# Optimization experiments

Hardware: AMD Instinct MI355X
Metric: run time of the kernel (lower is better)

## Reference

```python
import jax, jax.numpy as jnp
import numpy as np

B, T, C, H = 2, 2048, 1024, 16  # batch, seq (== block_size), n_embd, n_head
HD = C // H  # head dim


def setup_inputs() -> dict:
    key = jax.random.key(0)
    k1, k2, k3 = jax.random.split(key, 3)
    x = jax.random.normal(k1, (B, T, C), dtype=jnp.float32)
    w_attn = jax.random.normal(k2, (C, 3 * C), dtype=jnp.float32) * (1.0 / np.sqrt(C))
    b_attn = jnp.zeros((3 * C,), dtype=jnp.float32)
    w_proj = jax.random.normal(k3, (C, C), dtype=jnp.float32) * (1.0 / np.sqrt(C))
    b_proj = jnp.zeros((C,), dtype=jnp.float32)
    return {"x": x, "w_attn": w_attn, "b_attn": b_attn, "w_proj": w_proj, "b_proj": b_proj}


def reference(x, w_attn, b_attn, w_proj, b_proj):
    # qkv projection: [B,T,3C]
    qkv = x @ w_attn + b_attn
    q, k, v = jnp.split(qkv, 3, axis=-1)
    # -> [B,H,T,HD]
    def to_heads(t):
        return t.reshape(B, T, H, HD).transpose(0, 2, 1, 3)
    q, k, v = to_heads(q), to_heads(k), to_heads(v)
    scale = 1.0 / np.sqrt(HD).astype(np.float32)
    # att: [B,H,T,T]
    att = jnp.einsum("bhqd,bhkd->bhqk", q, k) * scale
    causal = jnp.tril(jnp.ones((T, T), dtype=bool))
    att = jnp.where(causal[None, None], att, -jnp.inf)
    att = jax.nn.softmax(att, axis=-1)
    # y: [B,H,T,HD] -> [B,T,C]
    y = jnp.einsum("bhqk,bhkd->bhqd", att, v)
    y = y.transpose(0, 2, 1, 3).reshape(B, T, C)
    return y @ w_proj + b_proj
```

## Files before the change

kernel.cpp:

```cpp
#include <hip/hip_runtime.h>
#include <stdint.h>

#define Bb 2
#define Tt 2048
#define Cc 1024
#define Hh 16
#define HD 64
#define C3 3072

typedef __bf16 bf16x8 __attribute__((ext_vector_type(8)));
typedef float  f32x4  __attribute__((ext_vector_type(4)));
typedef unsigned short u16;
typedef u16 u16x8 __attribute__((ext_vector_type(8)));
typedef u16 u16x4 __attribute__((ext_vector_type(4)));

#define SCALE2 0.18033688f

__device__ __forceinline__ u16 f2bf(float f) {
  union { float f; unsigned u; } v; v.f = f;
  return (u16)((v.u + 0x7fffu + ((v.u >> 16) & 1u)) >> 16);
}
__device__ __forceinline__ float bf2f(u16 a) {
  union { unsigned u; float f; } v; v.u = ((unsigned)a) << 16; return v.f;
}

__device__ __forceinline__ void gl2lds16(const void* g, void* s) {
  __builtin_amdgcn_global_load_lds(
      (__attribute__((address_space(1))) void*)(g),
      (__attribute__((address_space(3))) void*)(s), 16, 0, 0);
}

__device__ __forceinline__ bf16x8 ldb8(const u16* p) {
  return __builtin_bit_cast(bf16x8, *(const u16x8*)p);
}

template <int N>
__device__ __forceinline__ void vmwait() {
  asm volatile("s_waitcnt vmcnt(%0)" :: "n"(N) : "memory");
}
__device__ __forceinline__ void barrier_nodrain() {
  __builtin_amdgcn_s_barrier();
  __builtin_amdgcn_sched_barrier(0);
}

__global__ __launch_bounds__(256)
void prep_kernel(const float* __restrict__ x, const float* __restrict__ w_attn,
                 const float* __restrict__ w_proj, u16* __restrict__ xb,
                 u16* __restrict__ wat, u16* __restrict__ wpt) {
  __shared__ u16 tile[64][65];
  const int blk = blockIdx.x;
  const int tid = threadIdx.x;
  if (blk < 4096) {
    int i = blk * 256 + tid;
    float4 v = ((const float4*)x)[i];
    u16x4 o = { f2bf(v.x), f2bf(v.y), f2bf(v.z), f2bf(v.w) };
    ((u16x4*)xb)[i] = o;
    return;
  }
  const float* in; u16* out; int R, C, c0, r0;
  if (blk < 4096 + 768) {
    int t = blk - 4096;
    in = w_attn; out = wat; R = 1024; C = 3072;
    c0 = (t % 48) * 64; r0 = (t / 48) * 64;
  } else {
    int t = blk - 4864;
    in = w_proj; out = wpt; R = 1024; C = 1024;
    c0 = (t & 15) * 64; r0 = (t >> 4) * 64;
  }
  int xx = tid & 63, yy = tid >> 6;
  #pragma unroll
  for (int rr = yy; rr < 64; rr += 4)
    tile[rr][xx] = f2bf(in[(size_t)(r0 + rr) * C + c0 + xx]);
  __syncthreads();
  #pragma unroll
  for (int rr = yy; rr < 64; rr += 4)
    out[(size_t)(c0 + rr) * R + r0 + xx] = tile[xx][rr];
}

template <int MODE, int BN, int MINW>
__global__ __launch_bounds__(256, MINW)
void gemm_bt(const u16* __restrict__ A, const u16* __restrict__ Bt,
             const float* __restrict__ bias, void* __restrict__ Cout,
             u16* __restrict__ Vt, int M, int N, int K) {
  __shared__ u16 As[3][128 * 32];
  __shared__ u16 Bs[3][BN * 32];
  constexpr int JT = BN / 32;
  constexpr int NB = BN / 128 + 1;
  constexpr int L  = 2 + NB;
  const int tid = threadIdx.x;
  const int ln  = tid & 63;
  const int w   = tid >> 6;
  const int wm  = w >> 1, wn = w & 1;
  const int l15 = ln & 15, lq = ln >> 4;
  const int swz2 = (l15 >> 1) & 3;
  const int m0 = blockIdx.y * 128, n0 = blockIdx.x * BN;

  int aoff[2], boff[NB];
  #pragma unroll
  for (int i = 0; i < 2; ++i) {
    int s = i * 256 + tid;
    int row = s >> 2, cg = (s & 3) ^ ((s >> 3) & 3);
    aoff[i] = (m0 + row) * K + cg * 8;
  }
  #pragma unroll
  for (int i = 0; i < NB; ++i) {
    int s = i * 256 + tid;
    int row = s >> 2, cg = (s & 3) ^ ((s >> 3) & 3);
    boff[i] = (n0 + row) * K + cg * 8;
  }

  f32x4 acc[4][JT];
  #pragma unroll
  for (int i = 0; i < 4; ++i)
    #pragma unroll
    for (int j = 0; j < JT; ++j)
      acc[i][j] = (f32x4){0.f, 0.f, 0.f, 0.f};

  const int NK = K >> 5;

  auto STAGE = [&](int buf, int t) {
    const int k0 = t * 32;
    #pragma unroll
    for (int i = 0; i < 2; ++i)
      gl2lds16(A + aoff[i] + k0, (char*)As[buf] + (size_t)(i * 256 + w * 64) * 16);
    #pragma unroll
    for (int i = 0; i < NB; ++i)
      gl2lds16(Bt + boff[i] + k0, (char*)Bs[buf] + (size_t)(i * 256 + w * 64) * 16);
  };

  STAGE(0, 0);
  if (NK > 1) STAGE(1, 1);

  int cur = 0;
  for (int it = 0; it < NK; ++it) {
    if (it + 1 < NK) vmwait<L>(); else vmwait<0>();
    barrier_nodrain();
    if (it + 2 < NK) STAGE(cur == 0 ? 2 : cur - 1, it + 2);
    const u16* AsB = As[cur];
    const u16* BsB = Bs[cur];
    bf16x8 af[4], bfr[JT];
    #pragma unroll
    for (int i = 0; i < 4; ++i)
      af[i] = ldb8(&AsB[(wm * 64 + i * 16 + l15) * 32 + ((lq ^ swz2) * 8)]);
    #pragma unroll
    for (int j = 0; j < JT; ++j)
      bfr[j] = ldb8(&BsB[(wn * (BN / 2) + j * 16 + l15) * 32 + ((lq ^ swz2) * 8)]);
    #pragma unroll
    for (int i = 0; i < 4; ++i)
      #pragma unroll
      for (int j = 0; j < JT; ++j)
        acc[i][j] = __builtin_amdgcn_mfma_f32_16x16x32_bf16(af[i], bfr[j], acc[i][j], 0, 0, 0);
    cur = (cur == 2) ? 0 : cur + 1;
  }

  if (MODE == 1 && n0 >= 2048) {
    #pragma unroll
    for (int i = 0; i < 4; ++i) {
      int rowb = m0 + wm * 64 + i * 16 + lq * 4;
      int b_ = rowb >> 11, t0 = rowb & 2047;
      int tl = t0 & 63;
      int c = tl >> 4, ll = (tl >> 2) & 3;
      int pos0 = (c >> 1) * 32 + ll * 8 + (c & 1) * 4;
      size_t tdst = (size_t)(t0 & ~63) + pos0;
      #pragma unroll
      for (int j = 0; j < JT; ++j) {
        int col = n0 + wn * (BN / 2) + j * 16 + l15;
        int hd = col - 2048;
        float bsv = bias[col];
        u16x4 pk;
        #pragma unroll
        for (int r = 0; r < 4; ++r) pk[r] = f2bf(acc[i][j][r] + bsv);
        *(u16x4*)&Vt[(size_t)(b_ * 1024 + hd) * Tt + tdst] = pk;
      }
    }
  } else {
    const int ldc = (MODE == 1) ? 2048 : N;
    #pragma unroll
    for (int i = 0; i < 4; ++i) {
      int row = m0 + wm * 64 + i * 16 + lq * 4;
      #pragma unroll
      for (int j = 0; j < JT; ++j) {
        int col = n0 + wn * (BN / 2) + j * 16 + l15;
        float bsv = bias[col];
        #pragma unroll
        for (int r = 0; r < 4; ++r) {
          float v = acc[i][j][r] + bsv;
          if (MODE == 1) ((u16*)Cout)[(size_t)(row + r) * ldc + col] = f2bf(v);
          else           ((float*)Cout)[(size_t)(row + r) * ldc + col] = v;
        }
      }
    }
  }
}


__device__ __forceinline__ bf16x8 packp(const f32x4& a, const f32x4& b) {
  bf16x8 r;
  #pragma unroll
  for (int i = 0; i < 4; ++i) { r[i] = (__bf16)a[i]; r[i + 4] = (__bf16)b[i]; }
  return r;
}
__device__ __forceinline__ bf16x8 qscale(const u16* p) {
  u16x8 q = *(const u16x8*)p;
  u16x8 s;
  #pragma unroll
  for (int j = 0; j < 8; ++j) s[j] = f2bf(bf2f(q[j]) * SCALE2);
  return __builtin_bit_cast(bf16x8, s);
}

__device__ __forceinline__ void softmax_step(f32x4 (&t)[4], float& m, f32x4 (&o)[4],
                                             f32x4& lacc, bool maskDiag, int kk,
                                             int qg, int lq) {
  if (maskDiag) {
    #pragma unroll
    for (int i = 0; i < 4; ++i)
      #pragma unroll
      for (int r = 0; r < 4; ++r) {
        int kv = kk + i * 16 + lq * 4 + r;
        if (kv > qg) t[i][r] = -__builtin_inff();
      }
  }
  float a0 = fmaxf(fmaxf(t[0][0], t[0][1]), fmaxf(t[0][2], t[0][3]));
  float a1 = fmaxf(fmaxf(t[1][0], t[1][1]), fmaxf(t[1][2], t[1][3]));
  float a2 = fmaxf(fmaxf(t[2][0], t[2][1]), fmaxf(t[2][2], t[2][3]));
  float a3 = fmaxf(fmaxf(t[3][0], t[3][1]), fmaxf(t[3][2], t[3][3]));
  float mx = fmaxf(fmaxf(a0, a1), fmaxf(a2, a3));
  mx = fmaxf(mx, __shfl_xor(mx, 16));
#if __has_builtin(__builtin_amdgcn_permlane32_swap)
  {
    unsigned mu = __builtin_bit_cast(unsigned, mx);
    auto r2 = __builtin_amdgcn_permlane32_swap(mu, mu, false, false);
    mx = fmaxf(__builtin_bit_cast(float, (unsigned)r2[0]),
               __builtin_bit_cast(float, (unsigned)r2[1]));
  }
#else
  mx = fmaxf(mx, __shfl_xor(mx, 32));
#endif
  if (!__all(mx <= m + 8.0f)) {
    float mn = fmaxf(m, mx);
    float al = __builtin_amdgcn_exp2f(m - mn);
    m = mn;
    lacc[0] *= al;
    #pragma unroll
    for (int jd = 0; jd < 4; ++jd)
      #pragma unroll
      for (int r = 0; r < 4; ++r) o[jd][r] *= al;
  }
  #pragma unroll
  for (int i = 0; i < 4; ++i)
    #pragma unroll
    for (int r = 0; r < 4; ++r)
      t[i][r] = __builtin_amdgcn_exp2f(t[i][r] - m);
}

__global__ __launch_bounds__(256, 3)
void attn_fused(const u16* __restrict__ qk, const u16* __restrict__ vt,
                u16* __restrict__ y) {
  __shared__ u16 Ks[3][64 * 64];
  __shared__ u16 Vts[3][64 * 64];
  const int tid = threadIdx.x;
  const int ln = tid & 63, w = tid >> 6;
  const int l15 = ln & 15, lq = ln >> 4;
  const int swz = l15 & 7;
  const int bx = blockIdx.x;
  const int bh = bx & 31;
  const int h  = bh & 15, b = bh >> 4;
  const int rr_ = bx >> 8, g = (bx >> 5) & 7;
  const int qt = (rr_ == 0) ? 31 - g : (rr_ == 1) ? 16 + g : (rr_ == 2) ? 15 - g : g;
  const int q0w = qt * 64 + w * 16;

  const u16* qbase = qk + (size_t)(b * Tt) * 2048 + h * HD;
  const u16* kbase = qk + (size_t)(b * Tt) * 2048 + 1024 + h * HD;
  const u16* vbase = vt + (size_t)(b * 1024 + h * HD) * Tt;

  const int s0 = tid, s1 = 256 + tid;
  const int koff0 = (s0 >> 3) * 2048 + (((s0 & 7) ^ ((s0 >> 3) & 7)) * 8);
  const int koff1 = (s1 >> 3) * 2048 + (((s1 & 7) ^ ((s1 >> 3) & 7)) * 8);

  const u16* qrA = qbase + (size_t)(q0w + l15) * 2048;
  bf16x8 qA0 = qscale(qrA + lq * 8), qA1 = qscale(qrA + 32 + lq * 8);

  bf16x8 ones;
  #pragma unroll
  for (int j = 0; j < 8; ++j) ones[j] = (__bf16)1.0f;

  f32x4 o[4];
  #pragma unroll
  for (int j = 0; j < 4; ++j) o[j] = (f32x4){0, 0, 0, 0};
  f32x4 lacc = (f32x4){0, 0, 0, 0};
  float m = -__builtin_inff();
  const int qg = q0w + l15;
  const int nkv = qt + 1;

  auto STAGE = [&](int buf, int t) {
    const u16* ks = kbase + (size_t)(t * 64) * 2048;
    const u16* vs = vbase + t * 64;
    gl2lds16(ks + koff0, (char*)Ks[buf] + w * 1024);
    gl2lds16(ks + koff1, (char*)Ks[buf] + 4096 + w * 1024);
    gl2lds16(vs + koff0, (char*)Vts[buf] + w * 1024);
    gl2lds16(vs + koff1, (char*)Vts[buf] + 4096 + w * 1024);
  };

  STAGE(0, 0);
  if (nkv > 1) STAGE(1, 1);

  int cur = 0;
  for (int it = 0; it < nkv; ++it) {
    const int kk = it * 64;
    if (it + 1 < nkv) vmwait<4>(); else vmwait<0>();
    barrier_nodrain();
    if (it + 2 < nkv) STAGE(cur == 0 ? 2 : cur - 1, it + 2);
    const u16* KsB  = Ks[cur];
    const u16* VtsB = Vts[cur];

    f32x4 t[4];
    #pragma unroll
    for (int i = 0; i < 4; ++i) t[i] = (f32x4){0, 0, 0, 0};
    __builtin_amdgcn_s_setprio(1);
    #pragma unroll
    for (int i = 0; i < 4; ++i) {
      bf16x8 kf0 = ldb8(&KsB[(i * 16 + l15) * 64 + ((lq    ) ^ swz) * 8]);
      bf16x8 kf1 = ldb8(&KsB[(i * 16 + l15) * 64 + ((lq + 4) ^ swz) * 8]);
      t[i] = __builtin_amdgcn_mfma_f32_16x16x32_bf16(kf0, qA0, t[i], 0, 0, 0);
      t[i] = __builtin_amdgcn_mfma_f32_16x16x32_bf16(kf1, qA1, t[i], 0, 0, 0);
    }
    __builtin_amdgcn_s_setprio(0);

    softmax_step(t, m, o, lacc, it == nkv - 1, kk, qg, lq);
    bf16x8 p0 = packp(t[0], t[1]), p1 = packp(t[2], t[3]);

    __builtin_amdgcn_s_setprio(1);
    #pragma unroll
    for (int mf = 0; mf < 2; ++mf) {
      bf16x8 pbv = mf ? p1 : p0;
      lacc = __builtin_amdgcn_mfma_f32_16x16x32_bf16(ones, pbv, lacc, 0, 0, 0);
      #pragma unroll
      for (int jd = 0; jd < 4; ++jd) {
        int d = jd * 16 + l15;
        bf16x8 vf = ldb8(&VtsB[d * 64 + ((mf * 4 + lq) ^ swz) * 8]);
        o[jd] = __builtin_amdgcn_mfma_f32_16x16x32_bf16(vf, pbv, o[jd], 0, 0, 0);
      }
    }
    __builtin_amdgcn_s_setprio(0);
    cur = (cur == 2) ? 0 : cur + 1;
  }

  float inv = 1.f / lacc[0];
  const size_t ybase = (size_t)(b * Tt + q0w + l15) * Cc + h * HD;
  #pragma unroll
  for (int jd = 0; jd < 4; ++jd) {
    u16x4 pk;
    #pragma unroll
    for (int r = 0; r < 4; ++r) pk[r] = f2bf(o[jd][r] * inv);
    *(u16x4*)&y[ybase + jd * 16 + lq * 4] = pk;
  }
}

extern "C" void kernel_launch(void* const* d_in, const int* in_sizes, int n_in,
                              void* d_out, int out_size, void* d_ws, size_t ws_size,
                              hipStream_t stream) {
  const float* x      = (const float*)d_in[0];
  const float* w_attn = (const float*)d_in[1];
  const float* b_attn = (const float*)d_in[2];
  const float* w_proj = (const float*)d_in[3];
  const float* b_proj = (const float*)d_in[4];
  float* out = (float*)d_out;

  char* ws = (char*)d_ws;
  u16* xb  = (u16*)(ws + 0);
  u16* wat = (u16*)(ws + 8388608);
  u16* wpt = (u16*)(ws + 14680064);
  u16* qkb = (u16*)(ws + 16777216);
  u16* vtb = (u16*)(ws + 33554432);
  u16* yb  = (u16*)(ws + 41943040);

  prep_kernel<<<5120, 256, 0, stream>>>(x, w_attn, w_proj, xb, wat, wpt);
  gemm_bt<1, 128, 3><<<dim3(24, 32), 256, 0, stream>>>(xb, wat, b_attn, (void*)qkb, vtb, 4096, 3072, 1024);
  attn_fused<<<1024, 256, 0, stream>>>(qkb, vtb, yb);
  gemm_bt<0, 64, 4><<<dim3(16, 32), 256, 0, stream>>>(yb, wpt, b_proj, (void*)out, nullptr, 4096, 1024, 1024);
}
```

Baseline: 174.5 us.

## Widen attention KV tiles to 128 keys with double-buffered LDS staging

```diff
diff --git a/kernel.cpp b/kernel.cpp
--- a/kernel.cpp
+++ b/kernel.cpp
@@ -208,60 +208,15 @@
   return __builtin_bit_cast(bf16x8, s);
 }
 
-__device__ __forceinline__ void softmax_step(f32x4 (&t)[4], float& m, f32x4 (&o)[4],
-                                             f32x4& lacc, bool maskDiag, int kk,
-                                             int qg, int lq) {
-  if (maskDiag) {
-    #pragma unroll
-    for (int i = 0; i < 4; ++i)
-      #pragma unroll
-      for (int r = 0; r < 4; ++r) {
-        int kv = kk + i * 16 + lq * 4 + r;
-        if (kv > qg) t[i][r] = -__builtin_inff();
-      }
-  }
-  float a0 = fmaxf(fmaxf(t[0][0], t[0][1]), fmaxf(t[0][2], t[0][3]));
-  float a1 = fmaxf(fmaxf(t[1][0], t[1][1]), fmaxf(t[1][2], t[1][3]));
-  float a2 = fmaxf(fmaxf(t[2][0], t[2][1]), fmaxf(t[2][2], t[2][3]));
-  float a3 = fmaxf(fmaxf(t[3][0], t[3][1]), fmaxf(t[3][2], t[3][3]));
-  float mx = fmaxf(fmaxf(a0, a1), fmaxf(a2, a3));
-  mx = fmaxf(mx, __shfl_xor(mx, 16));
-#if __has_builtin(__builtin_amdgcn_permlane32_swap)
-  {
-    unsigned mu = __builtin_bit_cast(unsigned, mx);
-    auto r2 = __builtin_amdgcn_permlane32_swap(mu, mu, false, false);
-    mx = fmaxf(__builtin_bit_cast(float, (unsigned)r2[0]),
-               __builtin_bit_cast(float, (unsigned)r2[1]));
-  }
-#else
-  mx = fmaxf(mx, __shfl_xor(mx, 32));
-#endif
-  if (!__all(mx <= m + 8.0f)) {
-    float mn = fmaxf(m, mx);
-    float al = __builtin_amdgcn_exp2f(m - mn);
-    m = mn;
-    lacc[0] *= al;
-    #pragma unroll
-    for (int jd = 0; jd < 4; ++jd)
-      #pragma unroll
-      for (int r = 0; r < 4; ++r) o[jd][r] *= al;
-  }
-  #pragma unroll
-  for (int i = 0; i < 4; ++i)
-    #pragma unroll
-    for (int r = 0; r < 4; ++r)
-      t[i][r] = __builtin_amdgcn_exp2f(t[i][r] - m);
-}
-
-__global__ __launch_bounds__(256, 3)
+__global__ __launch_bounds__(256, 2)
 void attn_fused(const u16* __restrict__ qk, const u16* __restrict__ vt,
                 u16* __restrict__ y) {
-  __shared__ u16 Ks[3][64 * 64];
-  __shared__ u16 Vts[3][64 * 64];
+  __shared__ u16 Ks[2][128 * 64];
+  __shared__ u16 Vts[2][64 * 128];
   const int tid = threadIdx.x;
   const int ln = tid & 63, w = tid >> 6;
   const int l15 = ln & 15, lq = ln >> 4;
-  const int swz = l15 & 7;
+  const int swzK = l15 & 7;
   const int bx = blockIdx.x;
   const int bh = bx & 31;
   const int h  = bh & 15, b = bh >> 4;
@@ -273,9 +228,13 @@
   const u16* kbase = qk + (size_t)(b * Tt) * 2048 + 1024 + h * HD;
   const u16* vbase = vt + (size_t)(b * 1024 + h * HD) * Tt;
 
-  const int s0 = tid, s1 = 256 + tid;
-  const int koff0 = (s0 >> 3) * 2048 + (((s0 & 7) ^ ((s0 >> 3) & 7)) * 8);
-  const int koff1 = (s1 >> 3) * 2048 + (((s1 & 7) ^ ((s1 >> 3) & 7)) * 8);
+  int koff[4], voff[4];
+  #pragma unroll
+  for (int i = 0; i < 4; ++i) {
+    int s = i * 256 + tid;
+    koff[i] = (s >> 3) * 2048 + (((s & 7) ^ ((s >> 3) & 7)) * 8);
+    voff[i] = (s >> 4) * Tt + (((s & 15) ^ ((s >> 4) & 15)) * 8);
+  }
 
   const u16* qrA = qbase + (size_t)(q0w + l15) * 2048;
   bf16x8 qA0 = qscale(qrA + lq * 8), qA1 = qscale(qrA + 32 + lq * 8);
@@ -290,59 +249,105 @@
   f32x4 lacc = (f32x4){0, 0, 0, 0};
   float m = -__builtin_inff();
   const int qg = q0w + l15;
-  const int nkv = qt + 1;
+  const int nkv = (qt >> 1) + 1;
 
   auto STAGE = [&](int buf, int t) {
-    const u16* ks = kbase + (size_t)(t * 64) * 2048;
-    const u16* vs = vbase + t * 64;
-    gl2lds16(ks + koff0, (char*)Ks[buf] + w * 1024);
-    gl2lds16(ks + koff1, (char*)Ks[buf] + 4096 + w * 1024);
-    gl2lds16(vs + koff0, (char*)Vts[buf] + w * 1024);
-    gl2lds16(vs + koff1, (char*)Vts[buf] + 4096 + w * 1024);
+    const u16* ks = kbase + (size_t)(t * 128) * 2048;
+    const u16* vs = vbase + t * 128;
+    #pragma unroll
+    for (int i = 0; i < 4; ++i) {
+      gl2lds16(ks + koff[i], (char*)Ks[buf] + (size_t)(i * 256 + w * 64) * 16);
+      gl2lds16(vs + voff[i], (char*)Vts[buf] + (size_t)(i * 256 + w * 64) * 16);
+    }
   };
 
   STAGE(0, 0);
-  if (nkv > 1) STAGE(1, 1);
-
   int cur = 0;
   for (int it = 0; it < nkv; ++it) {
-    const int kk = it * 64;
-    if (it + 1 < nkv) vmwait<4>(); else vmwait<0>();
-    barrier_nodrain();
-    if (it + 2 < nkv) STAGE(cur == 0 ? 2 : cur - 1, it + 2);
+    const int kk = it * 128;
+    __syncthreads();
+    if (it + 1 < nkv) STAGE(cur ^ 1, it + 1);
     const u16* KsB  = Ks[cur];
     const u16* VtsB = Vts[cur];
 
-    f32x4 t[4];
-    #pragma unroll
-    for (int i = 0; i < 4; ++i) t[i] = (f32x4){0, 0, 0, 0};
+    f32x4 t[8];
+    #pragma unroll
+    for (int i = 0; i < 8; ++i) t[i] = (f32x4){0, 0, 0, 0};
     __builtin_amdgcn_s_setprio(1);
     #pragma unroll
-    for (int i = 0; i < 4; ++i) {
-      bf16x8 kf0 = ldb8(&KsB[(i * 16 + l15) * 64 + ((lq    ) ^ swz) * 8]);
-      bf16x8 kf1 = ldb8(&KsB[(i * 16 + l15) * 64 + ((lq + 4) ^ swz) * 8]);
+    for (int i = 0; i < 8; ++i) {
+      bf16x8 kf0 = ldb8(&KsB[(i * 16 + l15) * 64 + ((lq      ^ swzK) * 8)]);
+      bf16x8 kf1 = ldb8(&KsB[(i * 16 + l15) * 64 + (((lq + 4) ^ swzK) * 8)]);
       t[i] = __builtin_amdgcn_mfma_f32_16x16x32_bf16(kf0, qA0, t[i], 0, 0, 0);
       t[i] = __builtin_amdgcn_mfma_f32_16x16x32_bf16(kf1, qA1, t[i], 0, 0, 0);
     }
     __builtin_amdgcn_s_setprio(0);
 
-    softmax_step(t, m, o, lacc, it == nkv - 1, kk, qg, lq);
-    bf16x8 p0 = packp(t[0], t[1]), p1 = packp(t[2], t[3]);
+    if (it == nkv - 1) {
+      #pragma unroll
+      for (int i = 0; i < 8; ++i)
+        #pragma unroll
+        for (int r = 0; r < 4; ++r) {
+          int kv = kk + i * 16 + lq * 4 + r;
+          if (kv > qg) t[i][r] = -__builtin_inff();
+        }
+    }
+
+    float a0 = fmaxf(fmaxf(t[0][0], t[0][1]), fmaxf(t[0][2], t[0][3]));
+    float a1 = fmaxf(fmaxf(t[1][0], t[1][1]), fmaxf(t[1][2], t[1][3]));
+    float a2 = fmaxf(fmaxf(t[2][0], t[2][1]), fmaxf(t[2][2], t[2][3]));
+    float a3 = fmaxf(fmaxf(t[3][0], t[3][1]), fmaxf(t[3][2], t[3][3]));
+    float a4 = fmaxf(fmaxf(t[4][0], t[4][1]), fmaxf(t[4][2], t[4][3]));
+    float a5 = fmaxf(fmaxf(t[5][0], t[5][1]), fmaxf(t[5][2], t[5][3]));
+    float a6 = fmaxf(fmaxf(t[6][0], t[6][1]), fmaxf(t[6][2], t[6][3]));
+    float a7 = fmaxf(fmaxf(t[7][0], t[7][1]), fmaxf(t[7][2], t[7][3]));
+    float mx = fmaxf(fmaxf(fmaxf(a0, a1), fmaxf(a2, a3)),
+                     fmaxf(fmaxf(a4, a5), fmaxf(a6, a7)));
+    mx = fmaxf(mx, __shfl_xor(mx, 16));
+#if __has_builtin(__builtin_amdgcn_permlane32_swap)
+    {
+      unsigned mu = __builtin_bit_cast(unsigned, mx);
+      auto r2 = __builtin_amdgcn_permlane32_swap(mu, mu, false, false);
+      mx = fmaxf(__builtin_bit_cast(float, (unsigned)r2[0]),
+                 __builtin_bit_cast(float, (unsigned)r2[1]));
+    }
+#else
+    mx = fmaxf(mx, __shfl_xor(mx, 32));
+#endif
+
+    if (!__all(mx <= m + 8.0f)) {
+      float mn = fmaxf(m, mx);
+      float al = __builtin_amdgcn_exp2f(m - mn);
+      m = mn;
+      lacc[0] *= al;
+      #pragma unroll
+      for (int jd = 0; jd < 4; ++jd)
+        #pragma unroll
+        for (int r = 0; r < 4; ++r) o[jd][r] *= al;
+    }
+    #pragma unroll
+    for (int i = 0; i < 8; ++i)
+      #pragma unroll
+      for (int r = 0; r < 4; ++r)
+        t[i][r] = __builtin_amdgcn_exp2f(t[i][r] - m);
+
+    bf16x8 pk_[4];
+    #pragma unroll
+    for (int ks = 0; ks < 4; ++ks) pk_[ks] = packp(t[2 * ks], t[2 * ks + 1]);
 
     __builtin_amdgcn_s_setprio(1);
     #pragma unroll
-    for (int mf = 0; mf < 2; ++mf) {
-      bf16x8 pbv = mf ? p1 : p0;
-      lacc = __builtin_amdgcn_mfma_f32_16x16x32_bf16(ones, pbv, lacc, 0, 0, 0);
+    for (int ks = 0; ks < 4; ++ks) {
+      lacc = __builtin_amdgcn_mfma_f32_16x16x32_bf16(ones, pk_[ks], lacc, 0, 0, 0);
       #pragma unroll
       for (int jd = 0; jd < 4; ++jd) {
         int d = jd * 16 + l15;
-        bf16x8 vf = ldb8(&VtsB[d * 64 + ((mf * 4 + lq) ^ swz) * 8]);
-        o[jd] = __builtin_amdgcn_mfma_f32_16x16x32_bf16(vf, pbv, o[jd], 0, 0, 0);
+        bf16x8 vf = ldb8(&VtsB[d * 128 + (((ks * 4 + lq) ^ l15) * 8)]);
+        o[jd] = __builtin_amdgcn_mfma_f32_16x16x32_bf16(vf, pk_[ks], o[jd], 0, 0, 0);
       }
     }
     __builtin_amdgcn_s_setprio(0);
-    cur = (cur == 2) ? 0 : cur + 1;
+    cur ^= 1;
   }
 
   float inv = 1.f / lacc[0];
```

New measurement: 171.9 us. No clear change (-1.5%).
